# Performance work log

Measured on AMD Instinct MI355X. Metric: run time of the kernel, lower is better.

Reference implementation:

```python
import jax, jax.numpy as jnp
import numpy as np

B, L, V, D = 8, 128, 32000, 64
R1, R2, UP = 2 * D, 5 * D, 10 * D  # first_reduce, second_reduce, up_scale defaults


def pos_enc(seq_len, d, n=10000.0):
    # matches getPositionEncoding: P[k,2i]=sin(k/n^(2i/d)), P[k,2i+1]=cos(k/n^(2i/d))
    k = jnp.arange(seq_len, dtype=jnp.float32)[:, None]
    i = jnp.arange(d // 2, dtype=jnp.float32)[None, :]
    ang = k / (n ** (2.0 * i / d))
    return jnp.stack([jnp.sin(ang), jnp.cos(ang)], axis=-1).reshape(seq_len, d)


def setup_inputs() -> dict:
    key = jax.random.key(0)
    ks = jax.random.split(key, 20)

    def lin(k, out_f, in_f):
        bound = 1.0 / np.sqrt(in_f)
        k1, k2 = jax.random.split(k)
        W = jax.random.uniform(k1, (out_f, in_f), jnp.float32, -bound, bound)
        b = jax.random.uniform(k2, (out_f,), jnp.float32, -bound, bound)
        return W, b

    inp = {"x": jax.random.uniform(ks[0], (B, L, V), jnp.float32)}
    inp["W_emb"], inp["b_emb"] = lin(ks[1], D, V)
    inp["W_pos1"], inp["b_pos1"] = lin(ks[2], D, 2 * D)
    inp["W_red"], inp["b_red"] = lin(ks[3], R1, L * D)
    inp["W_pos2"], inp["b_pos2"] = lin(ks[4], R1, 2 * R1)
    inp["W_red2"], inp["b_red2"] = lin(ks[5], R2, L * R1)
    inp["W_pos3"], inp["b_pos3"] = lin(ks[6], R2, 2 * R2)
    inp["W_up1"], inp["b_up1"] = lin(ks[7], UP, R2)
    inp["W_up2"], inp["b_up2"] = lin(ks[8], V, UP)
    inp["W_fin"], inp["b_fin"] = lin(ks[9], 1, L)
    return inp


def reference(x, W_emb, b_emb, W_pos1, b_pos1, W_red, b_red, W_pos2, b_pos2,
              W_red2, b_red2, W_pos3, b_pos3, W_up1, b_up1, W_up2, b_up2,
              W_fin, b_fin):
    relu = jax.nn.relu
    P1 = pos_enc(L, 2 * D)   # [L, 2D]
    P2 = pos_enc(L, 2 * R1)  # [L, 2*R1]
    P3 = pos_enc(L, 2 * R2)  # [L, 2*R2]

    h = relu(x @ W_emb.T + b_emb)                       # [B, L, D]
    h = h + relu(P1 @ W_pos1.T + b_pos1)[None]          # learned sin pos emb

    # einsum('bij,bkm->bikj'): out[b,i,k,j] = h[b,i,j] * sum_m h[b,k,m]
    s = h.sum(-1)                                       # [B, L]
    h = (h[:, :, None, :] * s[:, None, :, None]).reshape(B, L, L * D)
    h = relu(h @ W_red.T + b_red)                       # [B, L, R1]
    h = h + relu(P2 @ W_pos2.T + b_pos2)[None]

    s = h.sum(-1)                                       # [B, L]
    h = (h[:, :, None, :] * s[:, None, :, None]).reshape(B, L, L * R1)
    h = relu(h @ W_red2.T + b_red2)                     # [B, L, R2]
    h = h + relu(P3 @ W_pos3.T + b_pos3)[None]

    h = relu(h @ W_up1.T + b_up1)                       # [B, L, UP]
    h = relu(h @ W_up2.T + b_up2)                       # [B, L, V]
    # transpose(1,2) then Linear(L->1), relu, squeeze
    out = relu(jnp.einsum('blv,l->bv', h, W_fin[0]) + b_fin[0])  # [B, V]
    return out
```

## Files before the change

### kernel.cpp

```cpp
#include <hip/hip_runtime.h>
#include <hip/hip_bf16.h>
#include <math.h>

#define B_  8
#define L_  128
#define V_  32000
#define D_  64
#define R1_ 128
#define R2_ 320
#define UP_ 640
#define SPLITS_ 50

typedef short bf16x8 __attribute__((ext_vector_type(8)));
typedef float f32x4 __attribute__((ext_vector_type(4)));

#define GLDS16(gp, lp)                                                         \
    __builtin_amdgcn_global_load_lds(                                          \
        (const __attribute__((address_space(1))) void*)(gp),                   \
        (__attribute__((address_space(3))) void*)(lp), 16, 0, 0)

static __device__ inline unsigned short f2bf(float x) {
    __hip_bfloat16 h = __float2bfloat16(x);
    return *reinterpret_cast<unsigned short*>(&h);
}

static __device__ inline void split1(float v, unsigned short& h, unsigned short& l) {
    unsigned short hb = f2bf(v);
    float hf = __uint_as_float(((unsigned int)hb) << 16);
    h = hb;
    l = f2bf(v - hf);
}

__global__ __launch_bounds__(320) void prep_all(const float* __restrict__ Wemb,
                                                unsigned short* __restrict__ Whb,
                                                unsigned short* __restrict__ Wlb,
                                                const float* __restrict__ Wup2,
                                                unsigned short* __restrict__ Wup2b,
                                                const float* __restrict__ W1,
                                                const float* __restrict__ b1,
                                                float* __restrict__ o1,
                                                const float* __restrict__ W2,
                                                const float* __restrict__ b2,
                                                float* __restrict__ o2,
                                                const float* __restrict__ W3,
                                                const float* __restrict__ b3,
                                                float* __restrict__ o3) {
    __shared__ float P[640];
    int bx = blockIdx.x, t = threadIdx.x;
    if (bx < 800) {
        int u = bx * 320 + t;
        int kb = u >> 6, row = u & 63;
        const float* s = Wemb + (size_t)row * 32000 + kb * 8;
        unsigned short h8[8], l8[8];
#pragma unroll
        for (int j = 0; j < 8; ++j) split1(s[j], h8[j], l8[j]);
        *(ushort4*)&Whb[(size_t)u * 8]     = *(ushort4*)&h8[0];
        *(ushort4*)&Whb[(size_t)u * 8 + 4] = *(ushort4*)&h8[4];
        *(ushort4*)&Wlb[(size_t)u * 8]     = *(ushort4*)&l8[0];
        *(ushort4*)&Wlb[(size_t)u * 8 + 4] = *(ushort4*)&l8[4];
    } else if (bx < 1184) {
        int id = bx - 800;
        int l = id & 127;
        int stage = id >> 7;
        const float* W = (stage == 0) ? W1 : (stage == 1) ? W2 : W3;
        const float* bias = (stage == 0) ? b1 : (stage == 1) ? b2 : b3;
        float* out = (stage == 0) ? o1 : (stage == 1) ? o2 : o3;
        int outF = (stage == 0) ? 64 : (stage == 1) ? 128 : 320;
        int dEnc = 2 * outF;
        for (int m = t; m < dEnc; m += 320) {
            int i = m >> 1;
            float ang = (float)l * powf(10000.0f, -2.0f * (float)i / (float)dEnc);
            P[m] = (m & 1) ? cosf(ang) : sinf(ang);
        }
        __syncthreads();
        if (t < outF) {
            float acc = bias[t];
            const float4* w = (const float4*)(W + (size_t)t * dEnc);
            for (int m4 = 0; m4 < dEnc / 4; ++m4) {
                float4 wv = w[m4];
                float4 pv = *(const float4*)&P[m4 * 4];
                acc = fmaf(pv.x, wv.x, acc);
                acc = fmaf(pv.y, wv.y, acc);
                acc = fmaf(pv.z, wv.z, acc);
                acc = fmaf(pv.w, wv.w, acc);
            }
            out[l * outF + t] = fmaxf(acc, 0.f);
        }
    } else {
        const int n4 = (V_ * UP_) / 4;
        int stride = 3200 * 320;
        for (int i = (bx - 1184) * 320 + t; i < n4; i += stride) {
            float4 v = ((const float4*)Wup2)[i];
            ushort4 o;
            o.x = f2bf(v.x); o.y = f2bf(v.y); o.z = f2bf(v.z); o.w = f2bf(v.w);
            ((ushort4*)Wup2b)[i] = o;
        }
    }
}

__global__ __launch_bounds__(256) void embA_mfma(const float* __restrict__ x,
                                                 const unsigned short* __restrict__ Whb,
                                                 const unsigned short* __restrict__ Wlb,
                                                 float* __restrict__ partA) {
    __shared__ short lds[16384];
    int t = threadIdx.x;
    int lane = t & 63, w = t >> 6;
    int ln = lane & 15, lg = lane >> 4;
    int rb = blockIdx.x, ks = blockIdx.y;
    int row0 = rb * 64;
    const float* xrow = x + (size_t)(row0 + w * 16 + ln) * 32000;

    f32x4 acc[4];
#pragma unroll
    for (int nt = 0; nt < 4; ++nt) acc[nt] = (f32x4){0.f, 0.f, 0.f, 0.f};

    float4 xc[4], xn[4];
    {
        int kb0 = (ks * 640) >> 3;
#pragma unroll
        for (int s = 0; s < 4; ++s) {
            int ubase = s * 256 + w * 64;
            const unsigned short* arr = (s < 2) ? Whb : Wlb;
            int uu = (s < 2) ? ubase : (ubase - 512);
            const char* gp = (const char*)arr + ((size_t)kb0 * 64 + uu + lane) * 16;
            char* lp = (char*)lds + ((s < 2) ? 0 : 8192) + uu * 16;
            GLDS16(gp, lp);
        }
        const float* bp = xrow + ks * 640 + lg * 8;
        xc[0] = ((const float4*)bp)[0];
        xc[1] = ((const float4*)bp)[1];
        xc[2] = ((const float4*)(bp + 32))[0];
        xc[3] = ((const float4*)(bp + 32))[1];
    }

#pragma unroll 2
    for (int ch = 0; ch < 10; ++ch) {
        __syncthreads();
        if (ch < 9) {
            int kb0 = (ks * 640 + (ch + 1) * 64) >> 3;
            int p = (ch + 1) & 1;
#pragma unroll
            for (int s = 0; s < 4; ++s) {
                int ubase = s * 256 + w * 64;
                const unsigned short* arr = (s < 2) ? Whb : Wlb;
                int uu = (s < 2) ? ubase : (ubase - 512);
                const char* gp = (const char*)arr + ((size_t)kb0 * 64 + uu + lane) * 16;
                char* lp = (char*)lds + p * 16384 + ((s < 2) ? 0 : 8192) + uu * 16;
                GLDS16(gp, lp);
            }
            const float* bp = xrow + ks * 640 + (ch + 1) * 64 + lg * 8;
            xn[0] = ((const float4*)bp)[0];
            xn[1] = ((const float4*)bp)[1];
            xn[2] = ((const float4*)(bp + 32))[0];
            xn[3] = ((const float4*)(bp + 32))[1];
        }
        bf16x8 ah[2], al[2];
#pragma unroll
        for (int kstep = 0; kstep < 2; ++kstep) {
            float f[8] = {xc[2 * kstep].x, xc[2 * kstep].y, xc[2 * kstep].z, xc[2 * kstep].w,
                          xc[2 * kstep + 1].x, xc[2 * kstep + 1].y, xc[2 * kstep + 1].z,
                          xc[2 * kstep + 1].w};
            unsigned short h8[8], l8[8];
#pragma unroll
            for (int j = 0; j < 8; ++j) split1(f[j], h8[j], l8[j]);
            ah[kstep] = *(bf16x8*)h8;
            al[kstep] = *(bf16x8*)l8;
        }
        const char* buf = (const char*)lds + (ch & 1) * 16384;
#pragma unroll
        for (int kstep = 0; kstep < 2; ++kstep) {
            int g = kstep * 4 + lg;
#pragma unroll
            for (int nt = 0; nt < 4; ++nt) {
                int nrow = nt * 16 + ln;
                bf16x8 bh = *(const bf16x8*)(buf + (g * 64 + nrow) * 16);
                bf16x8 bl = *(const bf16x8*)(buf + 8192 + (g * 64 + nrow) * 16);
                acc[nt] = __builtin_amdgcn_mfma_f32_16x16x32_bf16(ah[kstep], bh, acc[nt], 0, 0, 0);
                acc[nt] = __builtin_amdgcn_mfma_f32_16x16x32_bf16(ah[kstep], bl, acc[nt], 0, 0, 0);
                acc[nt] = __builtin_amdgcn_mfma_f32_16x16x32_bf16(al[kstep], bh, acc[nt], 0, 0, 0);
            }
        }
#pragma unroll
        for (int i = 0; i < 4; ++i) xc[i] = xn[i];
    }
#pragma unroll
    for (int nt = 0; nt < 4; ++nt)
#pragma unroll
        for (int r = 0; r < 4; ++r)
            partA[((size_t)ks * 1024 + row0 + w * 16 + lg * 4 + r) * 64 + nt * 16 + ln] =
                acc[nt][r];
}

__global__ __launch_bounds__(64) void reduceA_kernel(const float* __restrict__ partA,
                                                     const float* __restrict__ bemb,
                                                     const float* __restrict__ pe1,
                                                     float* __restrict__ h1,
                                                     float* __restrict__ s1) {
    int lane = threadIdx.x;
    int row = blockIdx.x * 4 + (lane >> 4);
    int d0 = (lane & 15) * 4;
    float4 v = *(const float4*)&bemb[d0];
#pragma unroll 10
    for (int s = 0; s < SPLITS_; ++s) {
        float4 p = *(const float4*)&partA[((size_t)s * 1024 + row) * 64 + d0];
        v.x += p.x; v.y += p.y; v.z += p.z; v.w += p.w;
    }
    float4 pe = *(const float4*)&pe1[(row & 127) * 64 + d0];
    v.x = fmaxf(v.x, 0.f) + pe.x;
    v.y = fmaxf(v.y, 0.f) + pe.y;
    v.z = fmaxf(v.z, 0.f) + pe.z;
    v.w = fmaxf(v.w, 0.f) + pe.w;
    *(float4*)&h1[row * 64 + d0] = v;
    float sum = v.x + v.y + v.z + v.w;
#pragma unroll
    for (int off = 8; off >= 1; off >>= 1) sum += __shfl_down(sum, off);
    if ((lane & 15) == 0) s1[row] = sum;
}

__global__ __launch_bounds__(256) void wr1_kernel(const float* __restrict__ Wred,
                                                  const float* __restrict__ s1,
                                                  float* __restrict__ Wr1) {
    __shared__ float ss[1024];
    __shared__ float pl[2048];
    int t = threadIdx.x, bb = blockIdx.x;
    for (int i = t; i < 1024; i += 256) ss[i] = s1[i];
    __syncthreads();
    int r = bb >> 1, jh = bb & 1;
    int jj = t & 31, ks = t >> 5;
    int j = jh * 32 + jj;
    float acc[8];
#pragma unroll
    for (int b = 0; b < 8; ++b) acc[b] = 0.f;
    const float* w = Wred + (size_t)r * 8192 + j;
#pragma unroll
    for (int kk = 0; kk < 16; ++kk) {
        int k = ks * 16 + kk;
        float wv = w[k * 64];
#pragma unroll
        for (int b = 0; b < 8; ++b) acc[b] = fmaf(ss[b * 128 + k], wv, acc[b]);
    }
#pragma unroll
    for (int b = 0; b < 8; ++b) pl[t * 8 + b] = acc[b];
    __syncthreads();
    int jj2 = t >> 3, b2 = t & 7;
    float sum = 0.f;
#pragma unroll
    for (int k2 = 0; k2 < 8; ++k2) sum += pl[(k2 * 32 + jj2) * 8 + b2];
    Wr1[((size_t)b2 * 128 + r) * 64 + jh * 32 + jj2] = sum;
}

__global__ __launch_bounds__(128) void h2_kernel(const float* __restrict__ h1,
                                                 const float* __restrict__ Wr1,
                                                 const float* __restrict__ bred,
                                                 const float* __restrict__ pe2,
                                                 float* __restrict__ h2,
                                                 float* __restrict__ s2) {
    __shared__ float hrow[64];
    __shared__ float red[2];
    int row = blockIdx.x;
    int b = row >> 7, i = row & 127;
    int r = threadIdx.x;
    if (r < 64) hrow[r] = h1[row * 64 + r];
    __syncthreads();
    float acc = bred[r];
    const float4* w = (const float4*)(Wr1 + ((size_t)b * 128 + r) * 64);
#pragma unroll
    for (int j4 = 0; j4 < 16; ++j4) {
        float4 wv = w[j4];
        float4 hv = *(const float4*)&hrow[j4 * 4];
        acc = fmaf(hv.x, wv.x, acc);
        acc = fmaf(hv.y, wv.y, acc);
        acc = fmaf(hv.z, wv.z, acc);
        acc = fmaf(hv.w, wv.w, acc);
    }
    float val = fmaxf(acc, 0.f) + pe2[i * 128 + r];
    h2[row * 128 + r] = val;
    float sum = val;
    for (int off = 32; off > 0; off >>= 1) sum += __shfl_down(sum, off);
    if ((r & 63) == 0) red[r >> 6] = sum;
    __syncthreads();
    if (r == 0) s2[row] = red[0] + red[1];
}

__global__ __launch_bounds__(256) void wr2_kernel(const float* __restrict__ Wred2,
                                                  const float* __restrict__ s2,
                                                  float* __restrict__ Wr2) {
    __shared__ float ss[1024];
    __shared__ float pl[2048];
    int t = threadIdx.x, r = blockIdx.x;
    for (int i = t; i < 1024; i += 256) ss[i] = s2[i];
    __syncthreads();
    int j = t & 127, ks = t >> 7;
    float acc[8];
#pragma unroll
    for (int b = 0; b < 8; ++b) acc[b] = 0.f;
    const float* w = Wred2 + (size_t)r * 16384 + j;
#pragma unroll 16
    for (int kk = 0; kk < 64; ++kk) {
        int k = ks * 64 + kk;
        float wv = w[k * 128];
#pragma unroll
        for (int b = 0; b < 8; ++b) acc[b] = fmaf(ss[b * 128 + k], wv, acc[b]);
    }
#pragma unroll
    for (int b = 0; b < 8; ++b) pl[t * 8 + b] = acc[b];
    __syncthreads();
#pragma unroll
    for (int ii = 0; ii < 4; ++ii) {
        int idx = t * 4 + ii;
        int j2 = idx >> 3, b2 = idx & 7;
        float sum = pl[j2 * 8 + b2] + pl[(128 + j2) * 8 + b2];
        Wr2[((size_t)b2 * 320 + r) * 128 + j2] = sum;
    }
}

__global__ __launch_bounds__(256) void h3h4_kernel(const float* __restrict__ h2,
                                                   const float* __restrict__ Wr2,
                                                   const float* __restrict__ bred2,
                                                   const float* __restrict__ pe3,
                                                   const float* __restrict__ Wup1,
                                                   const float* __restrict__ bup1,
                                                   unsigned short* __restrict__ h4b) {
    __shared__ float h2r[512];
    __shared__ float hsT[1280];
    int t = threadIdx.x;
    int row0 = blockIdx.x * 4;
    int b = row0 >> 7;
    h2r[t] = h2[(size_t)row0 * 128 + t];
    h2r[t + 256] = h2[(size_t)row0 * 128 + t + 256];
    __syncthreads();
    int i_ = row0 & 127;
    for (int r = t; r < 320; r += 256) {
        const float4* w = (const float4*)(Wr2 + ((size_t)b * 320 + r) * 128);
        float a0 = bred2[r], a1 = a0, a2 = a0, a3 = a0;
#pragma unroll
        for (int j4 = 0; j4 < 32; ++j4) {
            float4 wv = w[j4];
            float4 q0 = *(const float4*)&h2r[0 * 128 + j4 * 4];
            float4 q1 = *(const float4*)&h2r[1 * 128 + j4 * 4];
            float4 q2 = *(const float4*)&h2r[2 * 128 + j4 * 4];
            float4 q3 = *(const float4*)&h2r[3 * 128 + j4 * 4];
            a0 = fmaf(q0.x, wv.x, a0); a0 = fmaf(q0.y, wv.y, a0);
            a0 = fmaf(q0.z, wv.z, a0); a0 = fmaf(q0.w, wv.w, a0);
            a1 = fmaf(q1.x, wv.x, a1); a1 = fmaf(q1.y, wv.y, a1);
            a1 = fmaf(q1.z, wv.z, a1); a1 = fmaf(q1.w, wv.w, a1);
            a2 = fmaf(q2.x, wv.x, a2); a2 = fmaf(q2.y, wv.y, a2);
            a2 = fmaf(q2.z, wv.z, a2); a2 = fmaf(q2.w, wv.w, a2);
            a3 = fmaf(q3.x, wv.x, a3); a3 = fmaf(q3.y, wv.y, a3);
            a3 = fmaf(q3.z, wv.z, a3); a3 = fmaf(q3.w, wv.w, a3);
        }
        hsT[r * 4 + 0] = fmaxf(a0, 0.f) + pe3[(i_ + 0) * 320 + r];
        hsT[r * 4 + 1] = fmaxf(a1, 0.f) + pe3[(i_ + 1) * 320 + r];
        hsT[r * 4 + 2] = fmaxf(a2, 0.f) + pe3[(i_ + 2) * 320 + r];
        hsT[r * 4 + 3] = fmaxf(a3, 0.f) + pe3[(i_ + 3) * 320 + r];
    }
    __syncthreads();
    for (int u = t; u < 640; u += 256) {
        float acc[4] = {0.f, 0.f, 0.f, 0.f};
        const float4* w = (const float4*)(Wup1 + (size_t)u * 320);
#pragma unroll 2
        for (int j4 = 0; j4 < 80; ++j4) {
            float4 wv = w[j4];
#pragma unroll
            for (int e = 0; e < 4; ++e) {
                float wc = (e == 0) ? wv.x : (e == 1) ? wv.y : (e == 2) ? wv.z : wv.w;
                float4 hv = *(const float4*)&hsT[(j4 * 4 + e) * 4];
                acc[0] = fmaf(hv.x, wc, acc[0]);
                acc[1] = fmaf(hv.y, wc, acc[1]);
                acc[2] = fmaf(hv.z, wc, acc[2]);
                acc[3] = fmaf(hv.w, wc, acc[3]);
            }
        }
        float bias = bup1[u];
#pragma unroll
        for (int q = 0; q < 4; ++q)
            h4b[(size_t)(row0 + q) * 640 + u] = f2bf(fmaxf(acc[q] + bias, 0.f));
    }
}

__global__ __launch_bounds__(512) void final_mfma_kernel(
    const unsigned short* __restrict__ h4b,
    const unsigned short* __restrict__ Wup2b,
    const float* __restrict__ bup2,
    const float* __restrict__ Wfin,
    const float* __restrict__ bfin,
    float* __restrict__ out) {
    __shared__ short tile[2][12288];
    __shared__ float redbuf[2][2][128];

    int t = threadIdx.x;
    int lane = t & 63;
    int w = t >> 6;
    int wv = w >> 2;
    int wq = w & 3;
    int bl_ = wq >> 1, lh = wq & 1;
    int ln = lane & 15, lg = lane >> 4;
    int b0 = blockIdx.x * 2;
    int v0 = blockIdx.y * 128;

    f32x4 acc[4][4];
#pragma unroll
    for (int mt = 0; mt < 4; ++mt)
#pragma unroll
        for (int nt = 0; nt < 4; ++nt) acc[mt][nt] = (f32x4){0.f, 0.f, 0.f, 0.f};

    auto stage = [&](int ch, int p) {
#pragma unroll
        for (int s = 0; s < 3; ++s) {
            int F = (w * 3 + s) * 1024 + lane * 16;
            const char* gp;
            if (F < 8192) {
                int pr = F >> 7;
                int u = (F >> 4) & 7;
                int l = u ^ (pr & 7);
                int o = l >> 2, g = l & 3;
                gp = (const char*)Wup2b +
                     (((size_t)(v0 + 2 * pr + o)) * 640 + (size_t)(ch * 32 + g * 8)) * 2;
            } else {
                int FF = F - 8192;
                int pr = FF >> 7;
                int u = (FF >> 4) & 7;
                int l = u ^ (pr & 7);
                int region = l >> 2, g = l & 3;
                gp = (const char*)h4b +
                     (((size_t)(b0 + region) * 128 + pr) * 640 +
                      (size_t)(ch * 32 + g * 8)) * 2;
            }
            char* lp = (char*)&tile[p][0] + (w * 3 + s) * 1024;
            GLDS16(gp, lp);
        }
    };

    stage(0, 0);

#pragma unroll 2
    for (int ch = 0; ch < 20; ++ch) {
        __syncthreads();
        if (ch < 19) stage(ch + 1, (ch + 1) & 1);
        const char* buf = (const char*)&tile[ch & 1][0];
        bf16x8 aF[4], bF[4];
#pragma unroll
        for (int mt = 0; mt < 4; ++mt) {
            int rA = wv * 64 + mt * 16 + ln;
            int pr = rA >> 1;
            int unit = (((rA & 1) << 2) | lg) ^ (pr & 7);
            aF[mt] = *(const bf16x8*)(buf + pr * 128 + unit * 16);
        }
#pragma unroll
        for (int nt = 0; nt < 4; ++nt) {
            int rB = lh * 64 + nt * 16 + ln;
            int unit = ((bl_ << 2) | lg) ^ (rB & 7);
            bF[nt] = *(const bf16x8*)(buf + 8192 + rB * 128 + unit * 16);
        }
#pragma unroll
        for (int mt = 0; mt < 4; ++mt)
#pragma unroll
            for (int nt = 0; nt < 4; ++nt)
                acc[mt][nt] = __builtin_amdgcn_mfma_f32_16x16x32_bf16(
                    aF[mt], bF[nt], acc[mt][nt], 0, 0, 0);
    }

    float bfin0 = bfin[0];
#pragma unroll
    for (int mt = 0; mt < 4; ++mt) {
        float bu[4];
#pragma unroll
        for (int r = 0; r < 4; ++r)
            bu[r] = bup2[v0 + wv * 64 + mt * 16 + lg * 4 + r];
        float part[4] = {0.f, 0.f, 0.f, 0.f};
#pragma unroll
        for (int nt = 0; nt < 4; ++nt) {
            float wf = Wfin[lh * 64 + nt * 16 + ln];
#pragma unroll
            for (int r = 0; r < 4; ++r)
                part[r] += wf * fmaxf(acc[mt][nt][r] + bu[r], 0.f);
        }
#pragma unroll
        for (int off = 8; off >= 1; off >>= 1)
#pragma unroll
            for (int r = 0; r < 4; ++r) part[r] += __shfl_xor(part[r], off, 64);
        if (ln == 0) {
#pragma unroll
            for (int r = 0; r < 4; ++r)
                redbuf[bl_][lh][wv * 64 + mt * 16 + lg * 4 + r] = part[r];
        }
    }
    __syncthreads();
    if (t < 256) {
        int bb = t >> 7, v = t & 127;
        float vsum = redbuf[bb][0][v] + redbuf[bb][1][v] + bfin0;
        out[(size_t)(b0 + bb) * 32000 + v0 + v] = fmaxf(vsum, 0.f);
    }
}

extern "C" void kernel_launch(void* const* d_in, const int* in_sizes, int n_in,
                              void* d_out, int out_size, void* d_ws, size_t ws_size,
                              hipStream_t stream) {
    const float* x      = (const float*)d_in[0];
    const float* W_emb  = (const float*)d_in[1];
    const float* b_emb  = (const float*)d_in[2];
    const float* W_pos1 = (const float*)d_in[3];
    const float* b_pos1 = (const float*)d_in[4];
    const float* W_red  = (const float*)d_in[5];
    const float* b_red  = (const float*)d_in[6];
    const float* W_pos2 = (const float*)d_in[7];
    const float* b_pos2 = (const float*)d_in[8];
    const float* W_red2 = (const float*)d_in[9];
    const float* b_red2 = (const float*)d_in[10];
    const float* W_pos3 = (const float*)d_in[11];
    const float* b_pos3 = (const float*)d_in[12];
    const float* W_up1  = (const float*)d_in[13];
    const float* b_up1  = (const float*)d_in[14];
    const float* W_up2  = (const float*)d_in[15];
    const float* b_up2  = (const float*)d_in[16];
    const float* W_fin  = (const float*)d_in[17];
    const float* b_fin  = (const float*)d_in[18];
    float* out = (float*)d_out;

    float* ws  = (float*)d_ws;
    float* pe1 = ws;
    float* pe2 = pe1 + 8192;
    float* pe3 = pe2 + 16384;
    float* h1  = pe3 + 40960;
    float* s1  = h1 + 65536;
    float* Wr1 = s1 + 1024;
    float* h2  = Wr1 + 65536;
    float* s2  = h2 + 131072;
    float* Wr2 = s2 + 1024;
    float* h3  = Wr2 + 327680;
    unsigned short* h4b   = (unsigned short*)(h3 + 327680);
    unsigned short* Wup2b = (unsigned short*)((float*)h4b + 327680);
    float* after = (float*)Wup2b + 10240000;
    unsigned short* Whb = (unsigned short*)after;
    unsigned short* Wlb = Whb + 2048000;
    float* partA = (float*)(Wlb + 2048000);

    prep_all<<<dim3(4384), 320, 0, stream>>>(W_emb, Whb, Wlb, W_up2, Wup2b,
                                             W_pos1, b_pos1, pe1, W_pos2, b_pos2,
                                             pe2, W_pos3, b_pos3, pe3);
    embA_mfma<<<dim3(16, SPLITS_), 256, 0, stream>>>(x, Whb, Wlb, partA);
    reduceA_kernel<<<dim3(256), 64, 0, stream>>>(partA, b_emb, pe1, h1, s1);
    wr1_kernel<<<dim3(256), 256, 0, stream>>>(W_red, s1, Wr1);
    h2_kernel<<<dim3(1024), 128, 0, stream>>>(h1, Wr1, b_red, pe2, h2, s2);
    wr2_kernel<<<dim3(320), 256, 0, stream>>>(W_red2, s2, Wr2);
    h3h4_kernel<<<dim3(256), 256, 0, stream>>>(h2, Wr2, b_red2, pe3, W_up1,
                                               b_up1, h4b);
    final_mfma_kernel<<<dim3(4, 250), 512, 0, stream>>>(h4b, Wup2b, b_up2, W_fin,
                                                        b_fin, out);
}
```

Before: 447.3 us.

## Fuse W_up2 bf16 conversion into final MFMA kernel's tile staging

Drops the separate pass in prep_all that converted the whole fp32 W_up2 matrix to bf16 in workspace. The final GEMM kernel now loads fp32 W_up2 rows into registers, converts them to bf16, and writes them into the swizzled LDS tile. The h4b operand still uses async global-to-LDS loads, and the register prefetch is overlapped with the MFMA loop. This removes a large read-plus-write pass over the biggest weight and shrinks the prep grid. In exchange, each final block reads twice as many bytes for the A operand, and the four batch blocks sharing a V tile each reread it, relying on L2 to absorb the repeats.

```diff
diff --git a/kernel.cpp b/kernel.cpp
--- a/kernel.cpp
+++ b/kernel.cpp
@@ -34,8 +34,6 @@
 __global__ __launch_bounds__(320) void prep_all(const float* __restrict__ Wemb,
                                                 unsigned short* __restrict__ Whb,
                                                 unsigned short* __restrict__ Wlb,
-                                                const float* __restrict__ Wup2,
-                                                unsigned short* __restrict__ Wup2b,
                                                 const float* __restrict__ W1,
                                                 const float* __restrict__ b1,
                                                 float* __restrict__ o1,
@@ -58,7 +56,7 @@
         *(ushort4*)&Whb[(size_t)u * 8 + 4] = *(ushort4*)&h8[4];
         *(ushort4*)&Wlb[(size_t)u * 8]     = *(ushort4*)&l8[0];
         *(ushort4*)&Wlb[(size_t)u * 8 + 4] = *(ushort4*)&l8[4];
-    } else if (bx < 1184) {
+    } else {
         int id = bx - 800;
         int l = id & 127;
         int stage = id >> 7;
@@ -85,15 +83,6 @@
                 acc = fmaf(pv.w, wv.w, acc);
             }
             out[l * outF + t] = fmaxf(acc, 0.f);
-        }
-    } else {
-        const int n4 = (V_ * UP_) / 4;
-        int stride = 3200 * 320;
-        for (int i = (bx - 1184) * 320 + t; i < n4; i += stride) {
-            float4 v = ((const float4*)Wup2)[i];
-            ushort4 o;
-            o.x = f2bf(v.x); o.y = f2bf(v.y); o.z = f2bf(v.z); o.w = f2bf(v.w);
-            ((ushort4*)Wup2b)[i] = o;
         }
     }
 }
@@ -380,7 +369,7 @@
 
 __global__ __launch_bounds__(512) void final_mfma_kernel(
     const unsigned short* __restrict__ h4b,
-    const unsigned short* __restrict__ Wup2b,
+    const float* __restrict__ Wup2,
     const float* __restrict__ bup2,
     const float* __restrict__ Wfin,
     const float* __restrict__ bfin,
@@ -404,39 +393,46 @@
 #pragma unroll
         for (int nt = 0; nt < 4; ++nt) acc[mt][nt] = (f32x4){0.f, 0.f, 0.f, 0.f};
 
-    auto stage = [&](int ch, int p) {
-#pragma unroll
-        for (int s = 0; s < 3; ++s) {
-            int F = (w * 3 + s) * 1024 + lane * 16;
-            const char* gp;
-            if (F < 8192) {
-                int pr = F >> 7;
-                int u = (F >> 4) & 7;
-                int l = u ^ (pr & 7);
-                int o = l >> 2, g = l & 3;
-                gp = (const char*)Wup2b +
-                     (((size_t)(v0 + 2 * pr + o)) * 640 + (size_t)(ch * 32 + g * 8)) * 2;
-            } else {
-                int FF = F - 8192;
-                int pr = FF >> 7;
-                int u = (FF >> 4) & 7;
-                int l = u ^ (pr & 7);
-                int region = l >> 2, g = l & 3;
-                gp = (const char*)h4b +
-                     (((size_t)(b0 + region) * 128 + pr) * 640 +
-                      (size_t)(ch * 32 + g * 8)) * 2;
-            }
-            char* lp = (char*)&tile[p][0] + (w * 3 + s) * 1024;
+    int prA = t >> 3;
+    int lA = (t & 7) ^ (prA & 7);
+    const float* srcA =
+        Wup2 + (size_t)(v0 + 2 * prA + (lA >> 2)) * 640 + (lA & 3) * 8;
+
+    auto stageB = [&](int ch, int p) {
+#pragma unroll
+        for (int s = 0; s < 2; ++s) {
+            int q = w * 128 + s * 64 + lane;
+            int pr = q >> 3;
+            int l = (q & 7) ^ (pr & 7);
+            int region = l >> 2, g = l & 3;
+            const char* gp = (const char*)h4b +
+                (((size_t)(b0 + region) * 128 + pr) * 640 +
+                 (size_t)(ch * 32 + g * 8)) * 2;
+            char* lp = (char*)&tile[p][0] + 8192 + w * 2048 + s * 1024;
             GLDS16(gp, lp);
         }
     };
 
-    stage(0, 0);
+    {
+        float4 a0 = ((const float4*)srcA)[0];
+        float4 a1 = ((const float4*)srcA)[1];
+        stageB(0, 0);
+        unsigned short u8[8] = {f2bf(a0.x), f2bf(a0.y), f2bf(a0.z), f2bf(a0.w),
+                                f2bf(a1.x), f2bf(a1.y), f2bf(a1.z), f2bf(a1.w)};
+        *(ushort4*)(&tile[0][0] + t * 8)     = *(ushort4*)&u8[0];
+        *(ushort4*)(&tile[0][0] + t * 8 + 4) = *(ushort4*)&u8[4];
+    }
 
 #pragma unroll 2
     for (int ch = 0; ch < 20; ++ch) {
         __syncthreads();
-        if (ch < 19) stage(ch + 1, (ch + 1) & 1);
+        float4 aN0, aN1;
+        if (ch < 19) {
+            const float* s = srcA + (ch + 1) * 32;
+            aN0 = ((const float4*)s)[0];
+            aN1 = ((const float4*)s)[1];
+            stageB(ch + 1, (ch + 1) & 1);
+        }
         const char* buf = (const char*)&tile[ch & 1][0];
         bf16x8 aF[4], bF[4];
 #pragma unroll
@@ -458,6 +454,13 @@
             for (int nt = 0; nt < 4; ++nt)
                 acc[mt][nt] = __builtin_amdgcn_mfma_f32_16x16x32_bf16(
                     aF[mt], bF[nt], acc[mt][nt], 0, 0, 0);
+        if (ch < 19) {
+            int p = (ch + 1) & 1;
+            unsigned short u8[8] = {f2bf(aN0.x), f2bf(aN0.y), f2bf(aN0.z), f2bf(aN0.w),
+                                    f2bf(aN1.x), f2bf(aN1.y), f2bf(aN1.z), f2bf(aN1.w)};
+            *(ushort4*)(&tile[p][0] + t * 8)     = *(ushort4*)&u8[0];
+            *(ushort4*)(&tile[p][0] + t * 8 + 4) = *(ushort4*)&u8[4];
+        }
     }
 
     float bfin0 = bfin[0];
@@ -528,14 +531,13 @@
     float* s2  = h2 + 131072;
     float* Wr2 = s2 + 1024;
     float* h3  = Wr2 + 327680;
-    unsigned short* h4b   = (unsigned short*)(h3 + 327680);
-    unsigned short* Wup2b = (unsigned short*)((float*)h4b + 327680);
-    float* after = (float*)Wup2b + 10240000;
+    unsigned short* h4b = (unsigned short*)(h3 + 327680);
+    float* after = (float*)h4b + 327680;
     unsigned short* Whb = (unsigned short*)after;
     unsigned short* Wlb = Whb + 2048000;
     float* partA = (float*)(Wlb + 2048000);
 
-    prep_all<<<dim3(4384), 320, 0, stream>>>(W_emb, Whb, Wlb, W_up2, Wup2b,
+    prep_all<<<dim3(1184), 320, 0, stream>>>(W_emb, Whb, Wlb,
                                              W_pos1, b_pos1, pe1, W_pos2, b_pos2,
                                              pe2, W_pos3, b_pos3, pe3);
     embA_mfma<<<dim3(16, SPLITS_), 256, 0, stream>>>(x, Whb, Wlb, partA);
@@ -545,6 +547,6 @@
     wr2_kernel<<<dim3(320), 256, 0, stream>>>(W_red2, s2, Wr2);
     h3h4_kernel<<<dim3(256), 256, 0, stream>>>(h2, Wr2, b_red2, pe3, W_up1,
                                                b_up1, h4b);
-    final_mfma_kernel<<<dim3(4, 250), 512, 0, stream>>>(h4b, Wup2b, b_up2, W_fin,
+    final_mfma_kernel<<<dim3(4, 250), 512, 0, stream>>>(h4b, W_up2, b_up2, W_fin,
                                                         b_fin, out);
 }
```

After: 470.5 us. +5.2%, slower.

## Retile final GEMM to one batch per block with 256 threads

Applied to the files above, without the earlier changes.

The final up-projection kernel now gives each block a single batch element (128 rows of h4) instead of two. Blocks shrink from 512 to 256 threads with a smaller LDS tile, and the grid doubles along the batch axis. The h4 staging and swizzle now use the same paired-row layout as the weight tile. This trades Wup2 reuse, since each weight tile is now loaded by twice as many blocks, for more resident blocks and less LDS per block.

```diff
diff --git a/kernel.cpp b/kernel.cpp
--- a/kernel.cpp
+++ b/kernel.cpp
@@ -378,24 +378,23 @@
     }
 }
 
-__global__ __launch_bounds__(512) void final_mfma_kernel(
+__global__ __launch_bounds__(256, 4) void final_mfma_kernel(
     const unsigned short* __restrict__ h4b,
     const unsigned short* __restrict__ Wup2b,
     const float* __restrict__ bup2,
     const float* __restrict__ Wfin,
     const float* __restrict__ bfin,
     float* __restrict__ out) {
-    __shared__ short tile[2][12288];
-    __shared__ float redbuf[2][2][128];
+    __shared__ short tile[2][8192];
+    __shared__ float redbuf[2][128];
 
     int t = threadIdx.x;
     int lane = t & 63;
     int w = t >> 6;
-    int wv = w >> 2;
-    int wq = w & 3;
-    int bl_ = wq >> 1, lh = wq & 1;
+    int wv = w >> 1;
+    int lh = w & 1;
     int ln = lane & 15, lg = lane >> 4;
-    int b0 = blockIdx.x * 2;
+    int b = blockIdx.x;
     int v0 = blockIdx.y * 128;
 
     f32x4 acc[4][4];
@@ -406,27 +405,27 @@
 
     auto stage = [&](int ch, int p) {
 #pragma unroll
-        for (int s = 0; s < 3; ++s) {
-            int F = (w * 3 + s) * 1024 + lane * 16;
+        for (int s = 0; s < 4; ++s) {
+            int seg = w * 4 + s;
+            int q = seg * 64 + lane;
             const char* gp;
-            if (F < 8192) {
-                int pr = F >> 7;
-                int u = (F >> 4) & 7;
+            if (q < 512) {
+                int pr = q >> 3, u = q & 7;
                 int l = u ^ (pr & 7);
                 int o = l >> 2, g = l & 3;
                 gp = (const char*)Wup2b +
-                     (((size_t)(v0 + 2 * pr + o)) * 640 + (size_t)(ch * 32 + g * 8)) * 2;
+                     (((size_t)(v0 + 2 * pr + o)) * 640 +
+                      (size_t)(ch * 32 + g * 8)) * 2;
             } else {
-                int FF = F - 8192;
-                int pr = FF >> 7;
-                int u = (FF >> 4) & 7;
+                int q2 = q - 512;
+                int pr = q2 >> 3, u = q2 & 7;
                 int l = u ^ (pr & 7);
-                int region = l >> 2, g = l & 3;
+                int o = l >> 2, g = l & 3;
                 gp = (const char*)h4b +
-                     (((size_t)(b0 + region) * 128 + pr) * 640 +
+                     (((size_t)b * 128 + 2 * pr + o) * 640 +
                       (size_t)(ch * 32 + g * 8)) * 2;
             }
-            char* lp = (char*)&tile[p][0] + (w * 3 + s) * 1024;
+            char* lp = (char*)&tile[p][0] + seg * 1024;
             GLDS16(gp, lp);
         }
     };
@@ -449,8 +448,9 @@
 #pragma unroll
         for (int nt = 0; nt < 4; ++nt) {
             int rB = lh * 64 + nt * 16 + ln;
-            int unit = ((bl_ << 2) | lg) ^ (rB & 7);
-            bF[nt] = *(const bf16x8*)(buf + 8192 + rB * 128 + unit * 16);
+            int pr = rB >> 1;
+            int unit = (((rB & 1) << 2) | lg) ^ (pr & 7);
+            bF[nt] = *(const bf16x8*)(buf + 8192 + pr * 128 + unit * 16);
         }
 #pragma unroll
         for (int mt = 0; mt < 4; ++mt)
@@ -482,14 +482,13 @@
         if (ln == 0) {
 #pragma unroll
             for (int r = 0; r < 4; ++r)
-                redbuf[bl_][lh][wv * 64 + mt * 16 + lg * 4 + r] = part[r];
-        }
-    }
-    __syncthreads();
-    if (t < 256) {
-        int bb = t >> 7, v = t & 127;
-        float vsum = redbuf[bb][0][v] + redbuf[bb][1][v] + bfin0;
-        out[(size_t)(b0 + bb) * 32000 + v0 + v] = fmaxf(vsum, 0.f);
+                redbuf[lh][wv * 64 + mt * 16 + lg * 4 + r] = part[r];
+        }
+    }
+    __syncthreads();
+    if (t < 128) {
+        float vsum = redbuf[0][t] + redbuf[1][t] + bfin0;
+        out[(size_t)b * 32000 + v0 + t] = fmaxf(vsum, 0.f);
     }
 }
 
@@ -545,6 +544,6 @@
     wr2_kernel<<<dim3(320), 256, 0, stream>>>(W_red2, s2, Wr2);
     h3h4_kernel<<<dim3(256), 256, 0, stream>>>(h2, Wr2, b_red2, pe3, W_up1,
                                                b_up1, h4b);
-    final_mfma_kernel<<<dim3(4, 250), 512, 0, stream>>>(h4b, Wup2b, b_up2, W_fin,
+    final_mfma_kernel<<<dim3(8, 250), 256, 0, stream>>>(h4b, Wup2b, b_up2, W_fin,
                                                         b_fin, out);
 }
```

Measured after the change: 456.4 us. 2.0% more time.
